# Kernel tuning notes

Measured on AMD Instinct MI355X. Metric: run time of the kernel, lower is better.

## Reference

```python
import jax, jax.numpy as jnp
import numpy as np

LN_EPS = 1e-5  # haiku LayerNorm default

def setup_inputs() -> dict:
    key = jax.random.key(0)
    ks = jax.random.split(key, 4)
    batch, width, mid = 8192, 1024, 4096
    x = jax.random.normal(ks[0], (batch, 4, width), dtype=jnp.float32)
    W1 = jax.random.normal(ks[1], (4 * width, mid), dtype=jnp.float32) / np.sqrt(4 * width)
    b1 = jnp.zeros((mid,), dtype=jnp.float32)
    W2 = jax.random.normal(ks[2], (mid, width), dtype=jnp.float32) / np.sqrt(mid)
    b2 = jnp.zeros((width,), dtype=jnp.float32)
    ln_scale = jnp.ones((width,), dtype=jnp.float32)
    ln_offset = jnp.zeros((width,), dtype=jnp.float32)
    return {"x": x, "ln_scale": ln_scale, "ln_offset": ln_offset,
            "W1": W1, "b1": b1, "W2": W2, "b2": b2}

def _layer_norm(x, scale, offset):
    mu = jnp.mean(x, axis=-1, keepdims=True)
    var = jnp.var(x, axis=-1, keepdims=True)
    return (x - mu) * jax.lax.rsqrt(var + LN_EPS) * scale + offset

def reference(x, ln_scale, ln_offset, W1, b1, W2, b2):
    batch, four, width = x.shape  # four == 4 (structural symmetry axis)
    y = _layer_norm(x, ln_scale, ln_offset)
    # rolls[b, k, j, :] = y[b, (j + k) % 4, :]; reshape concatenates along j
    rolls = jnp.stack([jnp.roll(y, -k, axis=1) for k in range(4)], axis=1)
    rolls = rolls.reshape(batch, 4, 4 * width)
    h = jnp.einsum('bkf,fm->bkm', rolls, W1) + b1  # (batch, 4, mid)
    h = jax.nn.gelu(h)  # approximate (tanh) gelu, jax default
    out = jnp.einsum('bkm,mw->bkw', h, W2) + b2  # (batch, 4, width)
    return x + out
```

## Files before the change

kernel.cpp:

```cpp
#include <hip/hip_runtime.h>
#include <hip/hip_bf16.h>
#include <cstdint>
#include <cstddef>

typedef __bf16 bf16_t;
typedef __bf16 bf16x4_v __attribute__((ext_vector_type(4)));
typedef __bf16 bf16x8_v __attribute__((ext_vector_type(8)));
typedef float  f32x4_v  __attribute__((ext_vector_type(4)));

__device__ __forceinline__ void gll16(const void* g, void* l) {
  __builtin_amdgcn_global_load_lds(
      (const __attribute__((address_space(1))) void*)g,
      (__attribute__((address_space(3))) void*)l, 16, 0, 0);
}

#define BARRIER()  asm volatile("s_barrier" ::: "memory")
#define WAIT_VM(N) asm volatile("s_waitcnt vmcnt(" #N ")" ::: "memory")

__device__ __forceinline__ float gelu_tanh(float x) {
  float z = 0.79788456080286535588f * (x + 0.044715f * x * x * x);
  return x / (1.0f + __expf(-2.0f * z));
}

__global__ __launch_bounds__(256) void ln_kernel(
    const float* __restrict__ X, const float* __restrict__ sc,
    const float* __restrict__ off, bf16_t* __restrict__ Y)
{
  const int row = blockIdx.x;
  const int tid = threadIdx.x;
  const float4 v = *(const float4*)&X[(size_t)row * 1024 + tid * 4];
  float s  = v.x + v.y + v.z + v.w;
  float s2 = v.x * v.x + v.y * v.y + v.z * v.z + v.w * v.w;
#pragma unroll
  for (int m = 1; m < 64; m <<= 1) {
    s  += __shfl_xor(s, m);
    s2 += __shfl_xor(s2, m);
  }
  __shared__ float red[8];
  const int wid = tid >> 6;
  if ((tid & 63) == 0) { red[wid] = s; red[4 + wid] = s2; }
  __syncthreads();
  s  = red[0] + red[1] + red[2] + red[3];
  s2 = red[4] + red[5] + red[6] + red[7];
  const float mu  = s * (1.0f / 1024.0f);
  float var = s2 * (1.0f / 1024.0f) - mu * mu;
  var = fmaxf(var, 0.0f);
  const float rs = rsqrtf(var + 1e-5f);
  const float4 g = *(const float4*)&sc[tid * 4];
  const float4 o = *(const float4*)&off[tid * 4];
  bf16x4_v y;
  y[0] = (bf16_t)((v.x - mu) * rs * g.x + o.x);
  y[1] = (bf16_t)((v.y - mu) * rs * g.y + o.y);
  y[2] = (bf16_t)((v.z - mu) * rs * g.z + o.z);
  y[3] = (bf16_t)((v.w - mu) * rs * g.w + o.w);
  *(bf16x4_v*)&Y[(size_t)row * 1024 + tid * 4] = y;
}

__global__ __launch_bounds__(256) void transpose_kernel(
    const float* __restrict__ Win, bf16_t* __restrict__ Wt, int R, int C)
{
  __shared__ float t[32][33];
  const int tx = threadIdx.x & 31;
  const int ty = (threadIdx.x >> 5) << 2;
  const int r0 = blockIdx.y * 32;
  const int c0 = blockIdx.x * 32;
#pragma unroll
  for (int r = 0; r < 4; ++r)
    t[ty + r][tx] = Win[(size_t)(r0 + ty + r) * C + (c0 + tx)];
  __syncthreads();
#pragma unroll
  for (int r = 0; r < 4; ++r)
    Wt[(size_t)(c0 + ty + r) * R + (r0 + tx)] = (bf16_t)t[tx][ty + r];
}


#define RD_A(DST, IB)                                                         \
  _Pragma("unroll") for (int i4_ = 0; i4_ < 4; ++i4_) {                       \
    DST[i4_][0] = *(const bf16x8_v*)(Ab + arow + ((IB) + i4_) * 2048 + cs0);  \
    DST[i4_][1] = *(const bf16x8_v*)(Ab + arow + ((IB) + i4_) * 2048 + cs1);  \
  }

#define RD_B(DST, JB)                                                         \
  _Pragma("unroll") for (int j2_ = 0; j2_ < 2; ++j2_) {                       \
    DST[j2_][0] = *(const bf16x8_v*)(Bb + brow + ((JB) + j2_) * 2048 + cs0);  \
    DST[j2_][1] = *(const bf16x8_v*)(Bb + brow + ((JB) + j2_) * 2048 + cs1);  \
  }

#define MFMAQ(AV, BV, I0, J0)                                                 \
  __builtin_amdgcn_s_setprio(1);                                              \
  _Pragma("unroll") for (int i2_ = 0; i2_ < 4; ++i2_)                         \
  _Pragma("unroll") for (int j2_ = 0; j2_ < 2; ++j2_)                         \
  _Pragma("unroll") for (int kk_ = 0; kk_ < 2; ++kk_)                         \
    acc[(I0) + i2_][(J0) + j2_] = __builtin_amdgcn_mfma_f32_16x16x32_bf16(    \
        AV[i2_][kk_], BV[j2_][kk_], acc[(I0) + i2_][(J0) + j2_], 0, 0, 0);    \
  __builtin_amdgcn_s_setprio(0);

#define ISSUE_A(NB, F, Q)                                                     \
  gll16(Asrc + ((size_t)(Q) * 64 * 4096) + (size_t)(F) * 64,                  \
        (char*)(&As[NB][0]) + (Q) * 8192 + ldsdst)
#define ISSUE_B(NB, F, Q)                                                     \
  gll16(Bsrc + ((size_t)(Q) * 64 * 4096) +                                    \
            (MODE == 1 ? ((((F) * 64) + rolloff) & 4095) : ((F) * 64)),       \
        (char*)(&Bs[NB][0]) + (Q) * 8192 + ldsdst)

template<int MODE>
__global__ __launch_bounds__(512, 2) void gemm256_kernel(
    const bf16_t* __restrict__ Ag, const bf16_t* __restrict__ Bg,
    const float* __restrict__ bias, const float* __restrict__ Xres,
    void* __restrict__ Out, long rowbase)
{
  __shared__ __align__(16) bf16_t As[2][256 * 64];
  __shared__ __align__(16) bf16_t Bs[2][256 * 64];

  const int tid  = threadIdx.x;
  const int lane = tid & 63;
  const int wid  = tid >> 6;
  const int wm   = wid >> 2;
  const int wn   = wid & 3;

  const int nwgx = gridDim.x;
  const int nwg  = nwgx * gridDim.y;
  const int flat = blockIdx.y * nwgx + blockIdx.x;
  const int swz  = (flat & 7) * (nwg >> 3) + (flat >> 3);
  const int bm   = swz % nwgx;
  const int bnl  = swz / nwgx;

  int kgrp = 0, m0, rolloff = 0;
  if (MODE == 1) { kgrp = bnl >> 4; m0 = (bnl & 15) << 8; rolloff = ((4 - kgrp) & 3) << 10; }
  else           { m0 = bnl << 8; }

  const int trow = tid >> 3;
  const int scb  = (((tid & 7) ^ (trow & 7)) << 4);
  const bf16_t* Asrc = Ag + (size_t)(bm * 256 + trow) * 4096 + (scb >> 1);
  const bf16_t* Bsrc = Bg + (size_t)(m0 + trow) * 4096 + (scb >> 1);
  const int ldsdst = (wid << 10);

  const int arow = (wm * 128 + (lane & 15)) * 128;
  const int brow = (wn * 64  + (lane & 15)) * 128;
  const int cs0  = (((lane >> 4) << 4)     ) ^ ((lane & 7) << 4);
  const int cs1  = (((lane >> 4) << 4) | 64) ^ ((lane & 7) << 4);

  f32x4_v  acc[8][4] = {};
  bf16x8_v a03[4][2], a47[4][2], b01[2][2], b23[2][2];

  ISSUE_B(0, 0, 0); ISSUE_B(0, 0, 1); ISSUE_B(0, 0, 2); ISSUE_B(0, 0, 3);
  ISSUE_A(0, 0, 0); ISSUE_A(0, 0, 2); ISSUE_A(0, 0, 1); ISSUE_A(0, 0, 3);
  WAIT_VM(2);
  BARRIER();

  int cur = 0;
  for (int f = 0; f < 64; ++f) {
    const char* Ab = (const char*)(&As[cur][0]);
    const char* Bb = (const char*)(&Bs[cur][0]);
    const int  nb = cur ^ 1;
    const bool st = (f < 63);

    {
      RD_B(b01, 0);
      RD_A(a03, 0);
      if (st) { ISSUE_B(nb, f + 1, 0); ISSUE_B(nb, f + 1, 1); }
      BARRIER();
      MFMAQ(a03, b01, 0, 0);
      if (st) { WAIT_VM(2); } else { WAIT_VM(0); }
      BARRIER();
    }
    {
      RD_A(a47, 4);
      if (st) { ISSUE_B(nb, f + 1, 2); ISSUE_B(nb, f + 1, 3); }
      BARRIER();
      MFMAQ(a47, b01, 4, 0);
      BARRIER();
    }
    {
      RD_B(b23, 2);
      if (st) { ISSUE_A(nb, f + 1, 0); ISSUE_A(nb, f + 1, 2); }
      BARRIER();
      MFMAQ(a03, b23, 0, 2);
      BARRIER();
    }
    {
      if (st) { ISSUE_A(nb, f + 1, 1); ISSUE_A(nb, f + 1, 3); }
      BARRIER();
      MFMAQ(a47, b23, 4, 2);
      if (st) WAIT_VM(2);
      BARRIER();
    }
    cur = nb;
  }

  const int cb16 = lane & 15;
  const int r4   = (lane >> 4) << 2;
  if (MODE == 1) {
    bf16_t* H = (bf16_t*)Out;
#pragma unroll
    for (int j = 0; j < 4; ++j) {
      const int m = m0 + wn * 64 + j * 16 + cb16;
      const float bv = bias[m];
#pragma unroll
      for (int i = 0; i < 8; ++i) {
        const int browi = bm * 256 + wm * 128 + i * 16 + r4;
#pragma unroll
        for (int r = 0; r < 4; ++r) {
          float v = acc[i][j][r] + bv;
          H[((size_t)(browi + r) * 4 + kgrp) * 4096 + m] = (bf16_t)gelu_tanh(v);
        }
      }
    }
  } else {
    float* O = (float*)Out;
#pragma unroll
    for (int j = 0; j < 4; ++j) {
      const int w = m0 + wn * 64 + j * 16 + cb16;
      const float bv = bias[w];
#pragma unroll
      for (int i = 0; i < 8; ++i) {
        const long row = rowbase + bm * 256 + wm * 128 + i * 16 + r4;
#pragma unroll
        for (int r = 0; r < 4; ++r)
          O[(size_t)(row + r) * 1024 + w] =
              Xres[(size_t)(row + r) * 1024 + w] + acc[i][j][r] + bv;
      }
    }
  }
}

extern "C" void kernel_launch(void* const* d_in, const int* in_sizes, int n_in,
                              void* d_out, int out_size, void* d_ws, size_t ws_size,
                              hipStream_t stream)
{
  const float* x   = (const float*)d_in[0];
  const float* lns = (const float*)d_in[1];
  const float* lno = (const float*)d_in[2];
  const float* W1  = (const float*)d_in[3];
  const float* b1  = (const float*)d_in[4];
  const float* W2  = (const float*)d_in[5];
  const float* b2  = (const float*)d_in[6];
  float* out = (float*)d_out;

  char* ws = (char*)d_ws;
  const size_t W1OFF = (size_t)64 << 20;
  const size_t W2OFF = (size_t)96 << 20;
  const size_t HOFF  = (size_t)104 << 20;
  bf16_t* Y   = (bf16_t*)(ws);
  bf16_t* W1t = (bf16_t*)(ws + W1OFF);
  bf16_t* W2t = (bf16_t*)(ws + W2OFF);
  bf16_t* H   = (bf16_t*)(ws + HOFF);

  ln_kernel<<<32768, 256, 0, stream>>>(x, lns, lno, Y);
  transpose_kernel<<<dim3(128, 128), 256, 0, stream>>>(W1, W1t, 4096, 4096);
  transpose_kernel<<<dim3(32, 128), 256, 0, stream>>>(W2, W2t, 4096, 1024);

  const size_t per_row = (size_t)4 * 4096 * 2;
  long chunk = 8192;
  if (ws_size < HOFF + (size_t)8192 * per_row) {
    long maxb = (long)((ws_size - HOFF) / per_row);
    chunk = maxb & ~255L;
    if (chunk < 256) chunk = 256;
  }
  for (long b0 = 0; b0 < 8192; b0 += chunk) {
    const long cb = (8192 - b0 < chunk) ? (8192 - b0) : chunk;
    gemm256_kernel<1><<<dim3(cb / 256, 64), 512, 0, stream>>>(
        Y + (size_t)b0 * 4096, W1t, b1, nullptr, (void*)H, 0);
    gemm256_kernel<2><<<dim3((cb * 4) / 256, 4), 512, 0, stream>>>(
        H, W2t, b2, x, (void*)out, b0 * 4);
  }
}
```

Baseline: 1.546 ms.

## Switch GEMM inner loop to 32x32x16 MFMA with restructured LDS fragment reads

Replaces the 16x16x32 bf16 MFMA tiling (8x4 accumulators of 4 floats) with 32x32x16 MFMA (4x2 accumulators of 16 floats), loading all B fragments once per k-step and streaming A fragments in four phases. Global-to-LDS prefetch issue is regrouped so all B loads go in phase one and all A loads in phase two, with adjusted waitcnt values. The larger MFMA shape is meant to cut LDS read traffic per FLOP and instruction count. In exchange it changes the register layout and epilogue row mapping, and the new waitcnt and barrier placement could weaken load overlap.

```diff
diff --git a/kernel.cpp b/kernel.cpp
--- a/kernel.cpp
+++ b/kernel.cpp
@@ -6,7 +6,7 @@
 typedef __bf16 bf16_t;
 typedef __bf16 bf16x4_v __attribute__((ext_vector_type(4)));
 typedef __bf16 bf16x8_v __attribute__((ext_vector_type(8)));
-typedef float  f32x4_v  __attribute__((ext_vector_type(4)));
+typedef float  f32x16_v __attribute__((ext_vector_type(16)));
 
 __device__ __forceinline__ void gll16(const void* g, void* l) {
   __builtin_amdgcn_global_load_lds(
@@ -74,25 +74,26 @@
 }
 
 
-#define RD_A(DST, IB)                                                         \
-  _Pragma("unroll") for (int i4_ = 0; i4_ < 4; ++i4_) {                       \
-    DST[i4_][0] = *(const bf16x8_v*)(Ab + arow + ((IB) + i4_) * 2048 + cs0);  \
-    DST[i4_][1] = *(const bf16x8_v*)(Ab + arow + ((IB) + i4_) * 2048 + cs1);  \
-  }
-
-#define RD_B(DST, JB)                                                         \
-  _Pragma("unroll") for (int j2_ = 0; j2_ < 2; ++j2_) {                       \
-    DST[j2_][0] = *(const bf16x8_v*)(Bb + brow + ((JB) + j2_) * 2048 + cs0);  \
-    DST[j2_][1] = *(const bf16x8_v*)(Bb + brow + ((JB) + j2_) * 2048 + cs1);  \
-  }
-
-#define MFMAQ(AV, BV, I0, J0)                                                 \
+#define RD_A4(DST, I)                                                         \
+  DST[0] = *(const bf16x8_v*)(Ab + arow0 + (I) * 4096 + csk0);                \
+  DST[1] = *(const bf16x8_v*)(Ab + arow0 + (I) * 4096 + csk1);                \
+  DST[2] = *(const bf16x8_v*)(Ab + arow0 + (I) * 4096 + csk2);                \
+  DST[3] = *(const bf16x8_v*)(Ab + arow0 + (I) * 4096 + csk3);
+
+#define RD_B8()                                                               \
+  _Pragma("unroll") for (int j_ = 0; j_ < 2; ++j_) {                          \
+    bfrag[j_][0] = *(const bf16x8_v*)(Bb + brow0 + j_ * 4096 + csk0);         \
+    bfrag[j_][1] = *(const bf16x8_v*)(Bb + brow0 + j_ * 4096 + csk1);         \
+    bfrag[j_][2] = *(const bf16x8_v*)(Bb + brow0 + j_ * 4096 + csk2);         \
+    bfrag[j_][3] = *(const bf16x8_v*)(Bb + brow0 + j_ * 4096 + csk3);         \
+  }
+
+#define MFMA_PH(AV, I)                                                        \
   __builtin_amdgcn_s_setprio(1);                                              \
-  _Pragma("unroll") for (int i2_ = 0; i2_ < 4; ++i2_)                         \
-  _Pragma("unroll") for (int j2_ = 0; j2_ < 2; ++j2_)                         \
-  _Pragma("unroll") for (int kk_ = 0; kk_ < 2; ++kk_)                         \
-    acc[(I0) + i2_][(J0) + j2_] = __builtin_amdgcn_mfma_f32_16x16x32_bf16(    \
-        AV[i2_][kk_], BV[j2_][kk_], acc[(I0) + i2_][(J0) + j2_], 0, 0, 0);    \
+  _Pragma("unroll") for (int ks_ = 0; ks_ < 4; ++ks_)                         \
+  _Pragma("unroll") for (int j_ = 0; j_ < 2; ++j_)                            \
+    acc[I][j_] = __builtin_amdgcn_mfma_f32_32x32x16_bf16(                     \
+        AV[ks_], bfrag[j_][ks_], acc[I][j_], 0, 0, 0);                        \
   __builtin_amdgcn_s_setprio(0);
 
 #define ISSUE_A(NB, F, Q)                                                     \
@@ -135,13 +136,17 @@
   const bf16_t* Bsrc = Bg + (size_t)(m0 + trow) * 4096 + (scb >> 1);
   const int ldsdst = (wid << 10);
 
-  const int arow = (wm * 128 + (lane & 15)) * 128;
-  const int brow = (wn * 64  + (lane & 15)) * 128;
-  const int cs0  = (((lane >> 4) << 4)     ) ^ ((lane & 7) << 4);
-  const int cs1  = (((lane >> 4) << 4) | 64) ^ ((lane & 7) << 4);
-
-  f32x4_v  acc[8][4] = {};
-  bf16x8_v a03[4][2], a47[4][2], b01[2][2], b23[2][2];
+  const int arow0 = (wm * 128 + (lane & 31)) * 128;
+  const int brow0 = (wn * 64  + (lane & 31)) * 128;
+  const int lhalf = (lane >> 5) << 4;
+  const int lswz  = (lane & 7) << 4;
+  const int csk0  = (0 * 32 + lhalf) ^ lswz;
+  const int csk1  = (1 * 32 + lhalf) ^ lswz;
+  const int csk2  = (2 * 32 + lhalf) ^ lswz;
+  const int csk3  = (3 * 32 + lhalf) ^ lswz;
+
+  f32x16_v acc[4][2] = {};
+  bf16x8_v bfrag[2][4];
 
   ISSUE_B(0, 0, 0); ISSUE_B(0, 0, 1); ISSUE_B(0, 0, 2); ISSUE_B(0, 0, 3);
   ISSUE_A(0, 0, 0); ISSUE_A(0, 0, 2); ISSUE_A(0, 0, 1); ISSUE_A(0, 0, 3);
@@ -150,75 +155,83 @@
 
   int cur = 0;
   for (int f = 0; f < 64; ++f) {
-    const char* Ab = (const char*)(&As[cur][0]);
-    const char* Bb = (const char*)(&Bs[cur][0]);
+    const char* Ab = (const char*)&As[cur][0];
+    const char* Bb = (const char*)&Bs[cur][0];
     const int  nb = cur ^ 1;
     const bool st = (f < 63);
 
     {
-      RD_B(b01, 0);
-      RD_A(a03, 0);
-      if (st) { ISSUE_B(nb, f + 1, 0); ISSUE_B(nb, f + 1, 1); }
-      BARRIER();
-      MFMAQ(a03, b01, 0, 0);
-      if (st) { WAIT_VM(2); } else { WAIT_VM(0); }
-      BARRIER();
-    }
-    {
-      RD_A(a47, 4);
-      if (st) { ISSUE_B(nb, f + 1, 2); ISSUE_B(nb, f + 1, 3); }
-      BARRIER();
-      MFMAQ(a47, b01, 4, 0);
-      BARRIER();
-    }
-    {
-      RD_B(b23, 2);
-      if (st) { ISSUE_A(nb, f + 1, 0); ISSUE_A(nb, f + 1, 2); }
-      BARRIER();
-      MFMAQ(a03, b23, 0, 2);
-      BARRIER();
-    }
-    {
-      if (st) { ISSUE_A(nb, f + 1, 1); ISSUE_A(nb, f + 1, 3); }
-      BARRIER();
-      MFMAQ(a47, b23, 4, 2);
+      RD_B8();
+      bf16x8_v av[4];
+      RD_A4(av, 0);
+      if (st) { ISSUE_B(nb, f + 1, 0); ISSUE_B(nb, f + 1, 1);
+                ISSUE_B(nb, f + 1, 2); ISSUE_B(nb, f + 1, 3); }
+      BARRIER();
+      MFMA_PH(av, 0);
+      BARRIER();
+    }
+    {
+      bf16x8_v av[4];
+      RD_A4(av, 1);
+      if (st) { ISSUE_A(nb, f + 1, 0); ISSUE_A(nb, f + 1, 2);
+                ISSUE_A(nb, f + 1, 1); ISSUE_A(nb, f + 1, 3); }
+      BARRIER();
+      MFMA_PH(av, 1);
+      if (st) { WAIT_VM(8); } else { WAIT_VM(0); }
+      BARRIER();
+    }
+    {
+      bf16x8_v av[4];
+      RD_A4(av, 2);
+      BARRIER();
+      MFMA_PH(av, 2);
+      BARRIER();
+    }
+    {
+      bf16x8_v av[4];
+      RD_A4(av, 3);
+      BARRIER();
+      MFMA_PH(av, 3);
       if (st) WAIT_VM(2);
       BARRIER();
     }
     cur = nb;
   }
 
-  const int cb16 = lane & 15;
-  const int r4   = (lane >> 4) << 2;
+  const int colL = lane & 31;
+  const int rhi  = (lane >> 5) << 2;
   if (MODE == 1) {
     bf16_t* H = (bf16_t*)Out;
 #pragma unroll
-    for (int j = 0; j < 4; ++j) {
-      const int m = m0 + wn * 64 + j * 16 + cb16;
-      const float bv = bias[m];
-#pragma unroll
-      for (int i = 0; i < 8; ++i) {
-        const int browi = bm * 256 + wm * 128 + i * 16 + r4;
-#pragma unroll
-        for (int r = 0; r < 4; ++r) {
-          float v = acc[i][j][r] + bv;
-          H[((size_t)(browi + r) * 4 + kgrp) * 4096 + m] = (bf16_t)gelu_tanh(v);
+    for (int i = 0; i < 4; ++i) {
+#pragma unroll
+      for (int j = 0; j < 2; ++j) {
+        const int m = m0 + wn * 64 + j * 32 + colL;
+        const float bv = bias[m];
+#pragma unroll
+        for (int reg = 0; reg < 16; ++reg) {
+          const int rit = (reg & 3) + ((reg >> 2) << 3) + rhi;
+          const int row = bm * 256 + wm * 128 + i * 32 + rit;
+          float v = acc[i][j][reg] + bv;
+          H[((size_t)row * 4 + kgrp) * 4096 + m] = (bf16_t)gelu_tanh(v);
         }
       }
     }
   } else {
     float* O = (float*)Out;
 #pragma unroll
-    for (int j = 0; j < 4; ++j) {
-      const int w = m0 + wn * 64 + j * 16 + cb16;
-      const float bv = bias[w];
-#pragma unroll
-      for (int i = 0; i < 8; ++i) {
-        const long row = rowbase + bm * 256 + wm * 128 + i * 16 + r4;
-#pragma unroll
-        for (int r = 0; r < 4; ++r)
-          O[(size_t)(row + r) * 1024 + w] =
-              Xres[(size_t)(row + r) * 1024 + w] + acc[i][j][r] + bv;
+    for (int i = 0; i < 4; ++i) {
+#pragma unroll
+      for (int j = 0; j < 2; ++j) {
+        const int w = m0 + wn * 64 + j * 32 + colL;
+        const float bv = bias[w];
+#pragma unroll
+        for (int reg = 0; reg < 16; ++reg) {
+          const int rit = (reg & 3) + ((reg >> 2) << 3) + rhi;
+          const long row = rowbase + bm * 256 + wm * 128 + i * 32 + rit;
+          O[(size_t)row * 1024 + w] =
+              Xres[(size_t)row * 1024 + w] + acc[i][j][reg] + bv;
+        }
       }
     }
   }
```

New measurement: 1.501 ms. -3.0%, faster.
